# Performance work log

Hardware: AMD Instinct MI355X
Metric: run time of the kernel (lower is better)

The kernel has to match this reference:

```python
import jax, jax.numpy as jnp
import numpy as np


def setup_inputs() -> dict:
    key = jax.random.key(0)
    k1, k2 = jax.random.split(key)
    B, F_in, N, F_out = 4, 64, 8192, 64
    x = jax.random.normal(k1, (B, F_in, N), dtype=jnp.float32)
    stdv = 1.0 / np.sqrt(F_out)
    weight = jax.random.uniform(k2, (F_in, F_out), dtype=jnp.float32, minval=-stdv, maxval=stdv)
    return {"x": x, "weight": weight}


def reference(x, weight):
    # x: [B, F_in, N], weight: [F_in, F_out]
    x_t = jnp.transpose(x, (0, 2, 1))              # [B, N, F_in]
    support = jnp.einsum('bnf,fo->bno', x_t, weight)  # [B, N, F_out]
    adj = jnp.einsum('bnf,bfm->bnm', x_t, x)       # [B, N, N]
    adj = jax.nn.softmax(adj, axis=2)
    out = jnp.einsum('bnm,bmo->bno', adj, support) # [B, N, F_out]
    return jnp.transpose(out, (0, 2, 1))           # [B, F_out, N]
```

## Files before the change

kernel.cpp:

```cpp
#include <hip/hip_runtime.h>

#define BATCH 4
#define NPTS  8192
#define FDIM  64
#define BK    64
#define NT    (NPTS / BK)

typedef _Float16 half_t;
typedef half_t half8  __attribute__((ext_vector_type(8)));
typedef half_t half2v __attribute__((ext_vector_type(2)));
typedef float  f32x4  __attribute__((ext_vector_type(4)));
typedef float  f32x16 __attribute__((ext_vector_type(16)));
typedef unsigned uint4v __attribute__((ext_vector_type(4)));
typedef unsigned uint2v __attribute__((ext_vector_type(2)));

__device__ inline unsigned pkrtz(float a, float b) {
    return __builtin_bit_cast(unsigned, __builtin_amdgcn_cvt_pkrtz(a, b));
}
__device__ inline half2v h2(unsigned u) { return __builtin_bit_cast(half2v, u); }

__device__ inline uint2v plswap(unsigned a, unsigned b) {
    return __builtin_amdgcn_permlane32_swap(a, b, false, false);
}

__global__ __launch_bounds__(256) void prep_kernel(
    const float* __restrict__ x, const float* __restrict__ w,
    half_t* __restrict__ ka, half_t* __restrict__ vt, float* __restrict__ nrm)
{
    int t = threadIdx.x;
    if (blockIdx.x < 512) {
        __shared__ float wl[FDIM * 16];
        int ob  = blockIdx.x & 3;
        int nch = blockIdx.x >> 2;
        #pragma unroll
        for (int i = 0; i < 4; ++i) {
            int idx = i * 256 + t;
            wl[idx] = w[(idx >> 4) * FDIM + ob * 16 + (idx & 15)];
        }
        __syncthreads();

        int gid = nch * 256 + t;
        int b = gid >> 13;
        int n = gid & (NPTS - 1);
        const float* xb = x + (size_t)b * FDIM * NPTS + n;

        float acc[16];
        #pragma unroll
        for (int o = 0; o < 16; ++o) acc[o] = 0.0f;
        #pragma unroll
        for (int f = 0; f < FDIM; ++f) {
            float xv = xb[(size_t)f * NPTS];
            const f32x4* wr = (const f32x4*)&wl[f * 16];
            f32x4 w0 = wr[0], w1 = wr[1], w2 = wr[2], w3 = wr[3];
            acc[ 0] += xv * w0[0]; acc[ 1] += xv * w0[1];
            acc[ 2] += xv * w0[2]; acc[ 3] += xv * w0[3];
            acc[ 4] += xv * w1[0]; acc[ 5] += xv * w1[1];
            acc[ 6] += xv * w1[2]; acc[ 7] += xv * w1[3];
            acc[ 8] += xv * w2[0]; acc[ 9] += xv * w2[1];
            acc[10] += xv * w2[2]; acc[11] += xv * w2[3];
            acc[12] += xv * w3[0]; acc[13] += xv * w3[1];
            acc[14] += xv * w3[2]; acc[15] += xv * w3[3];
        }
        half_t* vb = vt + (size_t)b * FDIM * NPTS + (size_t)ob * 16 * NPTS + n;
        #pragma unroll
        for (int o = 0; o < 16; ++o)
            vb[(size_t)o * NPTS] = (half_t)acc[o];
    } else {
        int gid = (blockIdx.x - 512) * 256 + t;
        int b = gid >> 13;
        int n = gid & (NPTS - 1);
        const float* xb = x + (size_t)b * FDIM * NPTS + n;

        float nr = 0.0f;
        half_t* kab = ka + (size_t)(gid >> 6) * 4096 + (size_t)(gid & 63) * 8;
        #pragma unroll
        for (int f8 = 0; f8 < 8; ++f8) {
            half8 h;
            #pragma unroll
            for (int j = 0; j < 8; ++j) {
                float xv = xb[(size_t)(f8 * 8 + j) * NPTS];
                nr += xv * xv;
                h[j] = (half_t)xv;
            }
            *(half8*)(kab + f8 * 512) = h;
        }
        nrm[gid] = nr * 1.44269504f;
    }
}

template<int SPLIT>
__global__ __launch_bounds__(256, 2) void flash_kernel(
    const half_t* __restrict__ qk, const half_t* __restrict__ vt,
    const float* __restrict__ nrm, float* __restrict__ out,
    half_t* __restrict__ part, float* __restrict__ lbuf)
{
    constexpr int TPS   = NT / SPLIT;
    constexpr int TOTAL = BATCH * SPLIT * (NPTS / 256);

    __shared__ half_t vl[2][BK * FDIM];

    int t    = threadIdx.x;
    int lane = t & 63;
    int l31  = lane & 31;
    int hi   = lane >> 5;
    int w    = t >> 6;

    int blk0 = blockIdx.x;
    int blk  = (blk0 & 7) * (TOTAL / 8) + (blk0 >> 3);
    int qc   = blk & 31;
    int rest = blk >> 5;
    int s    = rest & (SPLIT - 1);
    int b    = rest / SPLIT;
    int qw   = qc * 256 + w * 64;

    const half_t* kg = qk + (size_t)b * NPTS * FDIM;
    const half_t* vg = vt + (size_t)b * FDIM * NPTS;

    const half_t* qgb = kg + (size_t)(qw >> 6) * 4096 + (size_t)l31 * 8;
    half8 qf[2][4];
    #pragma unroll
    for (int qt = 0; qt < 2; ++qt)
        #pragma unroll
        for (int c = 0; c < 4; ++c) {
            qf[qt][c] = *(const half8*)(qgb + (c*2 + hi) * 512 + qt * 256);
            qf[qt][c] = qf[qt][c] * (half_t)1.44269504f;
        }

    float m2[2];
    #pragma unroll
    for (int qt = 0; qt < 2; ++qt)
        m2[qt] = nrm[(size_t)b * NPTS + qw + qt*32 + l31];

    int r0 = t >> 3, g0 = t & 7;
    int r1 = r0 + 32;
    int li0 = r0 * FDIM + ((g0 ^ (r0 & 7)) * 8);
    int li1 = r1 * FDIM + ((g0 ^ (r1 & 7)) * 8);

    int kb0 = s * TPS * BK;
    half8 s2 = *(const half8*)(vg + (size_t)r0 * NPTS + kb0 + g0*8);
    half8 s3 = *(const half8*)(vg + (size_t)r1 * NPTS + kb0 + g0*8);

    half8 kf[2][4];
    {
        const half_t* kgb = kg + (size_t)(kb0 >> 6) * 4096 + (size_t)l31 * 8;
        #pragma unroll
        for (int ct = 0; ct < 2; ++ct)
            #pragma unroll
            for (int c = 0; c < 4; ++c)
                kf[ct][c] = *(const half8*)(kgb + (c*2 + hi) * 512 + ct * 256);
    }

    f32x16 O[2][2];
    #pragma unroll
    for (int ot = 0; ot < 2; ++ot)
        #pragma unroll
        for (int qt = 0; qt < 2; ++qt)
            #pragma unroll
            for (int r = 0; r < 16; ++r) O[ot][qt][r] = 0.0f;
    float lsum[2] = {0.0f, 0.0f};

    for (int tt = 0; tt < TPS; ++tt) {
        half_t* vlb = vl[tt & 1];
        *(half8*)(vlb + li0) = s2;
        *(half8*)(vlb + li1) = s3;
        if (tt + 1 < TPS) {
            int kb = kb0 + (tt + 1) * BK;
            s2 = *(const half8*)(vg + (size_t)r0 * NPTS + kb + g0*8);
            s3 = *(const half8*)(vg + (size_t)r1 * NPTS + kb + g0*8);
        }
        __syncthreads();

        const half_t* kgbn = kg + (size_t)((kb0 + (tt + 1) * BK) >> 6) * 4096 + (size_t)l31 * 8;

        f32x16 S[2][2];
        #pragma unroll
        for (int ct = 0; ct < 2; ++ct)
            #pragma unroll
            for (int r = 0; r < 16; ++r) { S[ct][0][r] = -m2[0]; S[ct][1][r] = -m2[1]; }
        #pragma unroll
        for (int ct = 0; ct < 2; ++ct)
            #pragma unroll
            for (int c = 0; c < 4; ++c) {
                S[ct][0] = __builtin_amdgcn_mfma_f32_32x32x16_f16(kf[ct][c], qf[0][c], S[ct][0], 0, 0, 0);
                S[ct][1] = __builtin_amdgcn_mfma_f32_32x32x16_f16(kf[ct][c], qf[1][c], S[ct][1], 0, 0, 0);
            }
        if (tt + 1 < TPS) {
            #pragma unroll
            for (int ct = 0; ct < 2; ++ct)
                #pragma unroll
                for (int c = 0; c < 4; ++c)
                    kf[ct][c] = *(const half8*)(kgbn + (c*2 + hi) * 512 + ct * 256);
        }

        #pragma unroll
        for (int ct = 0; ct < 2; ++ct) {
            unsigned pk[2][8];
            #pragma unroll
            for (int qt = 0; qt < 2; ++qt) {
                #pragma unroll
                for (int rr = 0; rr < 8; ++rr)
                    pk[qt][rr] = pkrtz(__builtin_amdgcn_exp2f(S[ct][qt][2*rr]),
                                       __builtin_amdgcn_exp2f(S[ct][qt][2*rr+1]));
                half2v s2v = ((h2(pk[qt][0]) + h2(pk[qt][1])) + (h2(pk[qt][2]) + h2(pk[qt][3])))
                           + ((h2(pk[qt][4]) + h2(pk[qt][5])) + (h2(pk[qt][6]) + h2(pk[qt][7])));
                lsum[qt] += (float)s2v[0] + (float)s2v[1];
            }

            #pragma unroll
            for (int ktl = 0; ktl < 2; ++ktl) {
                const int kt = ct * 2 + ktl, i0 = ktl * 4;
                half8 pb[2];
                #pragma unroll
                for (int qt = 0; qt < 2; ++qt) {
                    uint2v r02 = plswap(pk[qt][i0+0], pk[qt][i0+2]);
                    uint2v r13 = plswap(pk[qt][i0+1], pk[qt][i0+3]);
                    uint4v uu; uu[0] = r02[0]; uu[1] = r13[0]; uu[2] = r02[1]; uu[3] = r13[1];
                    pb[qt] = __builtin_bit_cast(half8, uu);
                }
                int vrow0 = l31, vrow1 = 32 + l31;
                half8 vf0 = *(const half8*)(vlb + vrow0 * FDIM + (((2*kt + hi) ^ (vrow0 & 7)) * 8));
                half8 vf1 = *(const half8*)(vlb + vrow1 * FDIM + (((2*kt + hi) ^ (vrow1 & 7)) * 8));
                O[0][0] = __builtin_amdgcn_mfma_f32_32x32x16_f16(vf0, pb[0], O[0][0], 0, 0, 0);
                O[0][1] = __builtin_amdgcn_mfma_f32_32x32x16_f16(vf0, pb[1], O[0][1], 0, 0, 0);
                O[1][0] = __builtin_amdgcn_mfma_f32_32x32x16_f16(vf1, pb[0], O[1][0], 0, 0, 0);
                O[1][1] = __builtin_amdgcn_mfma_f32_32x32x16_f16(vf1, pb[1], O[1][1], 0, 0, 0);
            }
        }
    }

    lsum[0] += __shfl_xor(lsum[0], 32);
    lsum[1] += __shfl_xor(lsum[1], 32);

    if constexpr (SPLIT == 1) {
        float inv[2] = {1.0f / lsum[0], 1.0f / lsum[1]};
        size_t ob = (size_t)b * FDIM * NPTS;
        #pragma unroll
        for (int qt = 0; qt < 2; ++qt)
            #pragma unroll
            for (int ot = 0; ot < 2; ++ot)
                #pragma unroll
                for (int r = 0; r < 16; ++r) {
                    int o = ot*32 + (r & 3) + 8*(r >> 2) + 4*hi;
                    out[ob + (size_t)o * NPTS + qw + qt*32 + l31] = O[ot][qt][r] * inv[qt];
                }
    } else {
        half_t* pbase = part + (size_t)(s * BATCH + b) * FDIM * NPTS;
        #pragma unroll
        for (int ot = 0; ot < 2; ++ot)
            #pragma unroll
            for (int r = 0; r < 16; ++r) {
                int o = ot*32 + (r & 3) + 8*(r >> 2) + 4*hi;
                half_t* po = pbase + (size_t)o * NPTS + qw + l31;
                po[0]  = (half_t)O[ot][0][r];
                po[32] = (half_t)O[ot][1][r];
            }
        if (hi == 0) {
            float* lb = lbuf + (size_t)(s * BATCH + b) * NPTS + qw;
            lb[l31]      = lsum[0];
            lb[32 + l31] = lsum[1];
        }
    }
}

template<int SPLIT>
__global__ __launch_bounds__(256) void combine_kernel(
    const half_t* __restrict__ part, const float* __restrict__ lbuf,
    float* __restrict__ out)
{
    int gid  = blockIdx.x * 256 + threadIdx.x;
    int q8   = gid & (NPTS/8 - 1);
    int rest = gid >> 10;
    int b    = rest >> 6;
    int o    = rest & 63;
    size_t ro = (size_t)rest * NPTS + (size_t)q8 * 8;

    float acc[8], ls[8];
    #pragma unroll
    for (int j = 0; j < 8; ++j) { acc[j] = 0.0f; ls[j] = 0.0f; }
    #pragma unroll
    for (int s = 0; s < SPLIT; ++s) {
        half8 pv = *(const half8*)(part + (size_t)(s * BATCH + b) * FDIM * NPTS
                                        + (size_t)o * NPTS + (size_t)q8 * 8);
        const float* lb = lbuf + (size_t)(s * BATCH + b) * NPTS + (size_t)q8 * 8;
        #pragma unroll
        for (int j = 0; j < 8; ++j) { acc[j] += (float)pv[j]; ls[j] += lb[j]; }
    }
    #pragma unroll
    for (int j = 0; j < 8; ++j) acc[j] /= ls[j];
    *(f32x4*)(out + ro)     = *(f32x4*)&acc[0];
    *(f32x4*)(out + ro + 4) = *(f32x4*)&acc[4];
}

extern "C" void kernel_launch(void* const* d_in, const int* in_sizes, int n_in,
                              void* d_out, int out_size, void* d_ws, size_t ws_size,
                              hipStream_t stream) {
    (void)in_sizes; (void)n_in; (void)out_size;
    const float* x = (const float*)d_in[0];
    const float* w = (const float*)d_in[1];
    float* out = (float*)d_out;

    const size_t qelems = (size_t)BATCH * NPTS * FDIM;
    half_t* ka = (half_t*)d_ws;
    half_t* vt = ka + qelems;
    float* nrm = (float*)((char*)d_ws + 2 * qelems * sizeof(half_t));
    half_t* part = (half_t*)(nrm + (size_t)BATCH * NPTS);

    const size_t part_elems = (size_t)BATCH * FDIM * NPTS;
    const size_t l_elems    = (size_t)BATCH * NPTS;
    const size_t base_bytes = 2 * qelems * sizeof(half_t) + (size_t)BATCH * NPTS * sizeof(float);
    const size_t per_split  = part_elems * sizeof(half_t) + l_elems * sizeof(float);

    int split = 1;
    if (ws_size >= base_bytes + 4 * per_split)      split = 4;
    else if (ws_size >= base_bytes + 2 * per_split) split = 2;
    float* lbuf = (float*)(part + (size_t)split * part_elems);

    prep_kernel<<<640, 256, 0, stream>>>(x, w, ka, vt, nrm);

    if (split == 4) {
        flash_kernel<4><<<512, 256, 0, stream>>>(ka, vt, nrm, out, part, lbuf);
        combine_kernel<4><<<(BATCH * FDIM * NPTS) / 8 / 256, 256, 0, stream>>>(part, lbuf, out);
    } else if (split == 2) {
        flash_kernel<2><<<256, 256, 0, stream>>>(ka, vt, nrm, out, part, lbuf);
        combine_kernel<2><<<(BATCH * FDIM * NPTS) / 8 / 256, 256, 0, stream>>>(part, lbuf, out);
    } else {
        flash_kernel<1><<<128, 256, 0, stream>>>(ka, vt, nrm, out, nullptr, nullptr);
    }
}
```

Before: 80.64 us.

## Pre-tile V into MFMA fragment layout and load it directly from global

The projection stage now writes V^T in a tiled layout that matches the MFMA operand fragments, so the attention kernel loads V fragments straight from global/L2 into registers. This removes the LDS staging of V, the double-buffered shared tile and the per-iteration __syncthreads. A dummy 56KB shared array with a never-taken store is added to pin occupancy at a fixed level. The trade-off is more global memory traffic per wave and higher load latency inside the loop, since each wave now reads V itself instead of sharing one LDS copy.

New measurement: 82.37 us. +2.1%, slower.

```diff
diff --git a/kernel.cpp b/kernel.cpp
--- a/kernel.cpp
+++ b/kernel.cpp
@@ -61,10 +61,11 @@
             acc[12] += xv * w3[0]; acc[13] += xv * w3[1];
             acc[14] += xv * w3[2]; acc[15] += xv * w3[3];
         }
-        half_t* vb = vt + (size_t)b * FDIM * NPTS + (size_t)ob * 16 * NPTS + n;
+        half_t* vb = vt + (size_t)b * FDIM * NPTS + (size_t)(n >> 6) * 4096
+                   + (size_t)((n >> 4) & 3) * 1024 + (n & 15);
         #pragma unroll
         for (int o = 0; o < 16; ++o)
-            vb[(size_t)o * NPTS] = (half_t)acc[o];
+            vb[(size_t)(ob * 16 + o) * 16] = (half_t)acc[o];
     } else {
         int gid = (blockIdx.x - 512) * 256 + t;
         int b = gid >> 13;
@@ -97,7 +98,7 @@
     constexpr int TPS   = NT / SPLIT;
     constexpr int TOTAL = BATCH * SPLIT * (NPTS / 256);
 
-    __shared__ half_t vl[2][BK * FDIM];
+    __shared__ half_t occupancy_pin[28 * 1024];
 
     int t    = threadIdx.x;
     int lane = t & 63;
@@ -106,6 +107,8 @@
     int w    = t >> 6;
 
     int blk0 = blockIdx.x;
+    if (blk0 == 0x7fffffff) occupancy_pin[t] = (half_t)0.0f;
+
     int blk  = (blk0 & 7) * (TOTAL / 8) + (blk0 >> 3);
     int qc   = blk & 31;
     int rest = blk >> 5;
@@ -131,14 +134,7 @@
     for (int qt = 0; qt < 2; ++qt)
         m2[qt] = nrm[(size_t)b * NPTS + qw + qt*32 + l31];
 
-    int r0 = t >> 3, g0 = t & 7;
-    int r1 = r0 + 32;
-    int li0 = r0 * FDIM + ((g0 ^ (r0 & 7)) * 8);
-    int li1 = r1 * FDIM + ((g0 ^ (r1 & 7)) * 8);
-
     int kb0 = s * TPS * BK;
-    half8 s2 = *(const half8*)(vg + (size_t)r0 * NPTS + kb0 + g0*8);
-    half8 s3 = *(const half8*)(vg + (size_t)r1 * NPTS + kb0 + g0*8);
 
     half8 kf[2][4];
     {
@@ -160,15 +156,13 @@
     float lsum[2] = {0.0f, 0.0f};
 
     for (int tt = 0; tt < TPS; ++tt) {
-        half_t* vlb = vl[tt & 1];
-        *(half8*)(vlb + li0) = s2;
-        *(half8*)(vlb + li1) = s3;
-        if (tt + 1 < TPS) {
-            int kb = kb0 + (tt + 1) * BK;
-            s2 = *(const half8*)(vg + (size_t)r0 * NPTS + kb + g0*8);
-            s3 = *(const half8*)(vg + (size_t)r1 * NPTS + kb + g0*8);
-        }
-        __syncthreads();
+        const half_t* vtile = vg + (size_t)((kb0 + tt * BK) >> 6) * 4096;
+        half8 vf[4][2];
+        #pragma unroll
+        for (int kt = 0; kt < 4; ++kt) {
+            vf[kt][0] = *(const half8*)(vtile + kt * 1024 + l31 * 16 + hi * 8);
+            vf[kt][1] = *(const half8*)(vtile + kt * 1024 + (32 + l31) * 16 + hi * 8);
+        }
 
         const half_t* kgbn = kg + (size_t)((kb0 + (tt + 1) * BK) >> 6) * 4096 + (size_t)l31 * 8;
 
@@ -217,13 +211,10 @@
                     uint4v uu; uu[0] = r02[0]; uu[1] = r13[0]; uu[2] = r02[1]; uu[3] = r13[1];
                     pb[qt] = __builtin_bit_cast(half8, uu);
                 }
-                int vrow0 = l31, vrow1 = 32 + l31;
-                half8 vf0 = *(const half8*)(vlb + vrow0 * FDIM + (((2*kt + hi) ^ (vrow0 & 7)) * 8));
-                half8 vf1 = *(const half8*)(vlb + vrow1 * FDIM + (((2*kt + hi) ^ (vrow1 & 7)) * 8));
-                O[0][0] = __builtin_amdgcn_mfma_f32_32x32x16_f16(vf0, pb[0], O[0][0], 0, 0, 0);
-                O[0][1] = __builtin_amdgcn_mfma_f32_32x32x16_f16(vf0, pb[1], O[0][1], 0, 0, 0);
-                O[1][0] = __builtin_amdgcn_mfma_f32_32x32x16_f16(vf1, pb[0], O[1][0], 0, 0, 0);
-                O[1][1] = __builtin_amdgcn_mfma_f32_32x32x16_f16(vf1, pb[1], O[1][1], 0, 0, 0);
+                O[0][0] = __builtin_amdgcn_mfma_f32_32x32x16_f16(vf[kt][0], pb[0], O[0][0], 0, 0, 0);
+                O[0][1] = __builtin_amdgcn_mfma_f32_32x32x16_f16(vf[kt][0], pb[1], O[0][1], 0, 0, 0);
+                O[1][0] = __builtin_amdgcn_mfma_f32_32x32x16_f16(vf[kt][1], pb[0], O[1][0], 0, 0, 0);
+                O[1][1] = __builtin_amdgcn_mfma_f32_32x32x16_f16(vf[kt][1], pb[1], O[1][1], 0, 0, 0);
             }
         }
     }
```
